# Kernel tuning notes

Hardware: AMD Instinct MI355X
Metric: run time of the kernel (lower is better)

## Reference

```python
import jax, jax.numpy as jnp
import numpy as np

SCALE = 64.0
MARGIN = 0.35
EPS = 1e-7


def setup_inputs() -> dict:
    key = jax.random.key(0)
    k1, k2, k3 = jax.random.split(key, 3)
    B, D, C = 1024, 128, 100000
    embeddings = jax.random.normal(k1, (B, D), dtype=jnp.float32)
    labels = jax.random.randint(k2, (B,), 0, C, dtype=jnp.int64)
    W = jax.random.normal(k3, (C, D), dtype=jnp.float32)
    return {"embeddings": embeddings, "labels": labels, "W": W}


def reference(embeddings, labels, W):
    # L2-normalize class weights along feature dim (torch F.normalize, p=2, dim=1)
    W_norm = W / jnp.clip(jnp.linalg.norm(W, axis=1, keepdims=True), 1e-12)
    # cosine logits [B, C]
    cos_theta = jnp.clip(embeddings @ W_norm.T, -1.0 + EPS, 1.0 - EPS)
    # subtract margin only at the target class (equivalent to one-hot scatter)
    B = cos_theta.shape[0]
    rows = jnp.arange(B)
    cos_m = cos_theta.at[rows, labels].add(-MARGIN)
    logits = SCALE * cos_m
    # softmax cross-entropy with integer labels, mean reduction
    logp = jax.nn.log_softmax(logits, axis=-1)
    nll = -logp[rows, labels]
    return jnp.mean(nll)
```

## Files before the change

### kernel.cpp

```cpp
#include <hip/hip_runtime.h>
#include <hip/hip_bf16.h>

typedef float f32x4 __attribute__((ext_vector_type(4)));

#define B_SZ 1024
#define D_SZ 128
#define C_SZ 100000
#define CPAD 100096
#define BM 128
#define BN 128
#define NG 64
#define NCT 782

#define SCALE_F   64.0f
#define MARGIN_F  0.35f
#define CLIP_F    (1.0f - 1e-7f)
#define LOG2E_F   1.4426950408889634f
#define S_LOG2E_F (64.0f * 1.4426950408889634f)

__device__ __forceinline__ void gload_lds16(const void* g, void* l) {
    __builtin_amdgcn_global_load_lds(
        (const __attribute__((address_space(1))) void*)g,
        (__attribute__((address_space(3))) void*)l, 16, 0, 0);
}

__global__ void norm_conv(const float* __restrict__ W, unsigned int* __restrict__ Wf8,
                          const float* __restrict__ E, unsigned int* __restrict__ Ef8) {
    const int b = blockIdx.x;
    if (b < 12512) {
        const int lane = threadIdx.x & 63;
        const int l32  = lane & 31;
        const int row  = b * 8 + ((threadIdx.x >> 6) << 1) + (lane >> 5);
        if (row < C_SZ) {
            float4 v = reinterpret_cast<const float4*>(W + (size_t)row * D_SZ)[l32];
            float ss = v.x * v.x + v.y * v.y + v.z * v.z + v.w * v.w;
            #pragma unroll
            for (int m = 1; m < 32; m <<= 1) ss += __shfl_xor(ss, m);
            float sc = 1.0f / fmaxf(sqrtf(ss), 1e-12f);
            int r = __builtin_amdgcn_cvt_pk_fp8_f32(v.x * sc, v.y * sc, 0, false);
            r     = __builtin_amdgcn_cvt_pk_fp8_f32(v.z * sc, v.w * sc, r, true);
            Wf8[(size_t)row * 32 + l32] = (unsigned int)r;
        } else {
            Wf8[(size_t)row * 32 + l32] = 0u;
        }
    } else {
        const int i = (b - 12512) * 256 + threadIdx.x;
        float4 v = reinterpret_cast<const float4*>(E)[i];
        int r = __builtin_amdgcn_cvt_pk_fp8_f32(v.x, v.y, 0, false);
        r     = __builtin_amdgcn_cvt_pk_fp8_f32(v.z, v.w, r, true);
        Ef8[i] = (unsigned int)r;
    }
}

__launch_bounds__(512, 3)
__global__ void gemm_lse(const unsigned char* __restrict__ Ef8,
                         const unsigned char* __restrict__ Wf8,
                         float* __restrict__ P) {
    __shared__ unsigned char sB[2][BN * D_SZ];
    __shared__ float rs[2][BM];

    const int tid  = threadIdx.x;
    const int wave = tid >> 6;
    const int lane = tid & 63;
    const int g4   = lane >> 4;
    const int l15  = lane & 15;
    const int wm   = wave >> 1;
    const int wn   = wave & 1;
    const int g    = blockIdx.x;
    const int bi   = blockIdx.y;

    const int T = (NCT - g + NG - 1) / NG;

    const char* wbase = reinterpret_cast<const char*>(Wf8);
    const int srcOff = ((tid >> 3) << 7) + ((((tid & 7) ^ ((tid >> 3) & 7))) << 4);
    const int ldsOff = wave << 10;

#define STAGE(TI, BUF)                                                         \
    {                                                                          \
        const char* _s = wbase + (size_t)(TI) * 16384 + srcOff;                \
        char* _d = reinterpret_cast<char*>(BUF) + ldsOff;                      \
        gload_lds16(_s,        _d);                                            \
        gload_lds16(_s + 8192, _d + 8192);                                     \
    }

    STAGE(g, sB[0]);

    long a[2][4];
    {
        const char* ebase = reinterpret_cast<const char*>(Ef8) + (size_t)bi * BM * 128;
        #pragma unroll
        for (int mi = 0; mi < 2; ++mi) {
            const char* pr = ebase + (wm * 32 + mi * 16 + l15) * 128 + g4 * 8;
            #pragma unroll
            for (int kk = 0; kk < 4; ++kk)
                a[mi][kk] = *reinterpret_cast<const long*>(pr + kk * 32);
        }
    }

    const int swz = (l15 & 7) << 4;
    int rowb[4];
    #pragma unroll
    for (int ni = 0; ni < 4; ++ni) rowb[ni] = (wn * 64 + ni * 16 + l15) << 7;
    int kb[4];
    #pragma unroll
    for (int kk = 0; kk < 4; ++kk) kb[kk] = (kk * 32 + g4 * 8) ^ swz;

    float rowsum[2][4] = {};

    __syncthreads();

    int cur = 0;
    for (int t = 0; t < T; ++t) {
        if (t + 1 < T) STAGE(g + (t + 1) * NG, sB[cur ^ 1]);

        const char* sBb = reinterpret_cast<const char*>(sB[cur]);
        f32x4 acc[2][4] = {};
        #pragma unroll
        for (int kk = 0; kk < 4; ++kk) {
            long b[4];
            #pragma unroll
            for (int ni = 0; ni < 4; ++ni)
                b[ni] = *reinterpret_cast<const long*>(sBb + rowb[ni] + kb[kk]);
            #pragma unroll
            for (int mi = 0; mi < 2; ++mi)
                #pragma unroll
                for (int ni = 0; ni < 4; ++ni)
                    acc[mi][ni] = __builtin_amdgcn_mfma_f32_16x16x32_fp8_fp8(
                        a[mi][kk], b[ni], acc[mi][ni], 0, 0, 0);
        }

        #pragma unroll
        for (int mi = 0; mi < 2; ++mi) {
            #pragma unroll
            for (int r = 0; r < 4; ++r) {
                float s0 = 0.0f;
                #pragma unroll
                for (int ni = 0; ni < 4; ++ni)
                    s0 += __builtin_amdgcn_exp2f(
                        fminf(fmaf(acc[mi][ni][r], S_LOG2E_F, -S_LOG2E_F), 0.0f));
                rowsum[mi][r] += s0;
            }
        }
        __syncthreads();
        cur ^= 1;
    }

    #pragma unroll
    for (int mi = 0; mi < 2; ++mi) {
        #pragma unroll
        for (int r = 0; r < 4; ++r) {
            float s = rowsum[mi][r];
            s += __shfl_xor(s, 1);
            s += __shfl_xor(s, 2);
            s += __shfl_xor(s, 4);
            s += __shfl_xor(s, 8);
            rowsum[mi][r] = s;
        }
    }
    if (l15 == 0) {
        #pragma unroll
        for (int mi = 0; mi < 2; ++mi)
            #pragma unroll
            for (int r = 0; r < 4; ++r)
                rs[wn][wm * 32 + mi * 16 + g4 * 4 + r] = rowsum[mi][r];
    }
    __syncthreads();
    if (tid < BM)
        P[(size_t)g * B_SZ + bi * BM + tid] = rs[0][tid] + rs[1][tid];
#undef STAGE
}

__global__ void row_fin(const float* __restrict__ P, const float* __restrict__ E,
                        const float* __restrict__ W, const int* __restrict__ lab,
                        float* __restrict__ nll) {
    __shared__ float red[256];
    __shared__ float red2[128];
    const int row = blockIdx.x;
    const int t   = threadIdx.x;

    red[t] = (t < NG) ? P[(size_t)t * B_SZ + row] : 0.0f;
    __syncthreads();
    #pragma unroll
    for (int off = 128; off > 0; off >>= 1) {
        if (t < off) red[t] += red[t + off];
        __syncthreads();
    }
    const float S = red[0];
    __syncthreads();

    const int lb = lab[row];
    if (t < 128) {
        const float w = W[(size_t)lb * D_SZ + t];
        const float e = E[(size_t)row * D_SZ + t];
        red[t]  = e * w;
        red2[t] = w * w;
    } else {
        red[t] = 0.0f;
    }
    __syncthreads();
    #pragma unroll
    for (int off = 64; off > 0; off >>= 1) {
        if (t < off) { red[t] += red[t + off]; red2[t] += red2[t + off]; }
        __syncthreads();
    }

    if (t == 0) {
        const float ct = red[0] / fmaxf(sqrtf(red2[0]), 1e-12f);
        const float cc = fminf(fmaxf(ct, -CLIP_F), CLIP_F);
        const float lt = SCALE_F * (cc - MARGIN_F);
        float Sadj = S - exp2f(fminf((SCALE_F * cc - SCALE_F) * LOG2E_F, 0.0f))
                       + exp2f((lt - SCALE_F) * LOG2E_F);
        nll[row] = SCALE_F + logf(Sadj) - lt;
    }
}

__global__ void mean_k(const float* __restrict__ nll, float* __restrict__ out) {
    __shared__ float part[16];
    const int t = threadIdx.x;
    float v = nll[t];
    #pragma unroll
    for (int m = 1; m < 64; m <<= 1) v += __shfl_xor(v, m);
    if ((t & 63) == 0) part[t >> 6] = v;
    __syncthreads();
    if (t < 16) {
        float u = part[t];
        #pragma unroll
        for (int m = 1; m < 16; m <<= 1) u += __shfl_xor(u, m);
        if (t == 0) out[0] = u * (1.0f / 1024.0f);
    }
}

extern "C" void kernel_launch(void* const* d_in, const int* in_sizes, int n_in,
                              void* d_out, int out_size, void* d_ws, size_t ws_size,
                              hipStream_t stream) {
    const float* E   = (const float*)d_in[0];
    const int*   lab = (const int*)d_in[1];
    const float* W   = (const float*)d_in[2];
    float*       out = (float*)d_out;

    char* ws = (char*)d_ws;
    unsigned int* Ef8 = (unsigned int*)ws;
    unsigned int* Wf8 = (unsigned int*)(ws + 131072);
    float*        P   = (float*)(ws + 131072 + 12812288);
    float*        nll = (float*)(ws + 131072 + 12812288 + 262144);

    norm_conv<<<dim3(12640),   256, 0, stream>>>(W, Wf8, E, Ef8);
    gemm_lse <<<dim3(NG, 8),   512, 0, stream>>>((const unsigned char*)Ef8,
                                                 (const unsigned char*)Wf8, P);
    row_fin  <<<dim3(B_SZ),    256, 0, stream>>>(P, E, W, lab, nll);
    mean_k   <<<dim3(1),      1024, 0, stream>>>(nll, out);
}
```

Measured before the change: 52.73 us.

## Double GEMM row tile to 256 and fold mean into row_fin via atomicAdd

Each gemm_lse block now covers 256 embedding rows instead of 128, using two sets of A fragments and accumulators. Each staged fp8 W tile therefore feeds twice as many MFMAs, and the W stream is re-read half as many times. NG doubles to 128 so the grid keeps enough blocks. The separate mean kernel is removed: out is zeroed in norm_conv and row_fin atomically adds each scaled nll, saving one launch at the cost of a nondeterministic summation order. The doubled accumulator and A-fragment state raises register pressure under the 512x3 launch bounds, which risks spills or lower occupancy.

```diff
diff --git a/kernel.cpp b/kernel.cpp
--- a/kernel.cpp
+++ b/kernel.cpp
@@ -7,9 +7,9 @@
 #define D_SZ 128
 #define C_SZ 100000
 #define CPAD 100096
-#define BM 128
+#define BM 256
 #define BN 128
-#define NG 64
+#define NG 128
 #define NCT 782
 
 #define SCALE_F   64.0f
@@ -25,7 +25,8 @@
 }
 
 __global__ void norm_conv(const float* __restrict__ W, unsigned int* __restrict__ Wf8,
-                          const float* __restrict__ E, unsigned int* __restrict__ Ef8) {
+                          const float* __restrict__ E, unsigned int* __restrict__ Ef8,
+                          float* __restrict__ out) {
     const int b = blockIdx.x;
     if (b < 12512) {
         const int lane = threadIdx.x & 63;
@@ -44,6 +45,7 @@
             Wf8[(size_t)row * 32 + l32] = 0u;
         }
     } else {
+        if (b == 12512 && threadIdx.x == 0) out[0] = 0.0f;
         const int i = (b - 12512) * 256 + threadIdx.x;
         float4 v = reinterpret_cast<const float4*>(E)[i];
         int r = __builtin_amdgcn_cvt_pk_fp8_f32(v.x, v.y, 0, false);
@@ -85,16 +87,18 @@
 
     STAGE(g, sB[0]);
 
-    long a[2][4];
+    long a[2][2][4];
     {
         const char* ebase = reinterpret_cast<const char*>(Ef8) + (size_t)bi * BM * 128;
         #pragma unroll
-        for (int mi = 0; mi < 2; ++mi) {
-            const char* pr = ebase + (wm * 32 + mi * 16 + l15) * 128 + g4 * 8;
-            #pragma unroll
-            for (int kk = 0; kk < 4; ++kk)
-                a[mi][kk] = *reinterpret_cast<const long*>(pr + kk * 32);
-        }
+        for (int h = 0; h < 2; ++h)
+            #pragma unroll
+            for (int mi = 0; mi < 2; ++mi) {
+                const char* pr = ebase + (h * 128 + wm * 32 + mi * 16 + l15) * 128 + g4 * 8;
+                #pragma unroll
+                for (int kk = 0; kk < 4; ++kk)
+                    a[h][mi][kk] = *reinterpret_cast<const long*>(pr + kk * 32);
+            }
     }
 
     const int swz = (l15 & 7) << 4;
@@ -105,7 +109,7 @@
     #pragma unroll
     for (int kk = 0; kk < 4; ++kk) kb[kk] = (kk * 32 + g4 * 8) ^ swz;
 
-    float rowsum[2][4] = {};
+    float rowsum[2][2][4] = {};
 
     __syncthreads();
 
@@ -114,7 +118,7 @@
         if (t + 1 < T) STAGE(g + (t + 1) * NG, sB[cur ^ 1]);
 
         const char* sBb = reinterpret_cast<const char*>(sB[cur]);
-        f32x4 acc[2][4] = {};
+        f32x4 acc[2][2][4] = {};
         #pragma unroll
         for (int kk = 0; kk < 4; ++kk) {
             long b[4];
@@ -122,47 +126,54 @@
             for (int ni = 0; ni < 4; ++ni)
                 b[ni] = *reinterpret_cast<const long*>(sBb + rowb[ni] + kb[kk]);
             #pragma unroll
+            for (int h = 0; h < 2; ++h)
+                #pragma unroll
+                for (int mi = 0; mi < 2; ++mi)
+                    #pragma unroll
+                    for (int ni = 0; ni < 4; ++ni)
+                        acc[h][mi][ni] = __builtin_amdgcn_mfma_f32_16x16x32_fp8_fp8(
+                            a[h][mi][kk], b[ni], acc[h][mi][ni], 0, 0, 0);
+        }
+
+        #pragma unroll
+        for (int h = 0; h < 2; ++h)
+            #pragma unroll
             for (int mi = 0; mi < 2; ++mi)
                 #pragma unroll
-                for (int ni = 0; ni < 4; ++ni)
-                    acc[mi][ni] = __builtin_amdgcn_mfma_f32_16x16x32_fp8_fp8(
-                        a[mi][kk], b[ni], acc[mi][ni], 0, 0, 0);
-        }
-
-        #pragma unroll
-        for (int mi = 0; mi < 2; ++mi) {
-            #pragma unroll
-            for (int r = 0; r < 4; ++r) {
-                float s0 = 0.0f;
-                #pragma unroll
-                for (int ni = 0; ni < 4; ++ni)
-                    s0 += __builtin_amdgcn_exp2f(
-                        fminf(fmaf(acc[mi][ni][r], S_LOG2E_F, -S_LOG2E_F), 0.0f));
-                rowsum[mi][r] += s0;
-            }
-        }
+                for (int r = 0; r < 4; ++r) {
+                    float s0 = 0.0f;
+                    #pragma unroll
+                    for (int ni = 0; ni < 4; ++ni)
+                        s0 += __builtin_amdgcn_exp2f(
+                            fminf(fmaf(acc[h][mi][ni][r], S_LOG2E_F, -S_LOG2E_F), 0.0f));
+                    rowsum[h][mi][r] += s0;
+                }
+
         __syncthreads();
         cur ^= 1;
     }
 
     #pragma unroll
-    for (int mi = 0; mi < 2; ++mi) {
-        #pragma unroll
-        for (int r = 0; r < 4; ++r) {
-            float s = rowsum[mi][r];
-            s += __shfl_xor(s, 1);
-            s += __shfl_xor(s, 2);
-            s += __shfl_xor(s, 4);
-            s += __shfl_xor(s, 8);
-            rowsum[mi][r] = s;
-        }
-    }
+    for (int h = 0; h < 2; ++h)
+        #pragma unroll
+        for (int mi = 0; mi < 2; ++mi)
+            #pragma unroll
+            for (int r = 0; r < 4; ++r) {
+                float s = rowsum[h][mi][r];
+                s += __shfl_xor(s, 1);
+                s += __shfl_xor(s, 2);
+                s += __shfl_xor(s, 4);
+                s += __shfl_xor(s, 8);
+                rowsum[h][mi][r] = s;
+            }
     if (l15 == 0) {
         #pragma unroll
-        for (int mi = 0; mi < 2; ++mi)
-            #pragma unroll
-            for (int r = 0; r < 4; ++r)
-                rs[wn][wm * 32 + mi * 16 + g4 * 4 + r] = rowsum[mi][r];
+        for (int h = 0; h < 2; ++h)
+            #pragma unroll
+            for (int mi = 0; mi < 2; ++mi)
+                #pragma unroll
+                for (int r = 0; r < 4; ++r)
+                    rs[wn][h * 128 + wm * 32 + mi * 16 + g4 * 4 + r] = rowsum[h][mi][r];
     }
     __syncthreads();
     if (tid < BM)
@@ -172,7 +183,7 @@
 
 __global__ void row_fin(const float* __restrict__ P, const float* __restrict__ E,
                         const float* __restrict__ W, const int* __restrict__ lab,
-                        float* __restrict__ nll) {
+                        float* __restrict__ out) {
     __shared__ float red[256];
     __shared__ float red2[128];
     const int row = blockIdx.x;
@@ -210,23 +221,7 @@
         const float lt = SCALE_F * (cc - MARGIN_F);
         float Sadj = S - exp2f(fminf((SCALE_F * cc - SCALE_F) * LOG2E_F, 0.0f))
                        + exp2f((lt - SCALE_F) * LOG2E_F);
-        nll[row] = SCALE_F + logf(Sadj) - lt;
-    }
-}
-
-__global__ void mean_k(const float* __restrict__ nll, float* __restrict__ out) {
-    __shared__ float part[16];
-    const int t = threadIdx.x;
-    float v = nll[t];
-    #pragma unroll
-    for (int m = 1; m < 64; m <<= 1) v += __shfl_xor(v, m);
-    if ((t & 63) == 0) part[t >> 6] = v;
-    __syncthreads();
-    if (t < 16) {
-        float u = part[t];
-        #pragma unroll
-        for (int m = 1; m < 16; m <<= 1) u += __shfl_xor(u, m);
-        if (t == 0) out[0] = u * (1.0f / 1024.0f);
+        atomicAdd(out, (SCALE_F + logf(Sadj) - lt) * (1.0f / 1024.0f));
     }
 }
 
@@ -242,11 +237,9 @@
     unsigned int* Ef8 = (unsigned int*)ws;
     unsigned int* Wf8 = (unsigned int*)(ws + 131072);
     float*        P   = (float*)(ws + 131072 + 12812288);
-    float*        nll = (float*)(ws + 131072 + 12812288 + 262144);
-
-    norm_conv<<<dim3(12640),   256, 0, stream>>>(W, Wf8, E, Ef8);
-    gemm_lse <<<dim3(NG, 8),   512, 0, stream>>>((const unsigned char*)Ef8,
+
+    norm_conv<<<dim3(12640),   256, 0, stream>>>(W, Wf8, E, Ef8, out);
+    gemm_lse <<<dim3(NG, 4),   512, 0, stream>>>((const unsigned char*)Ef8,
                                                  (const unsigned char*)Wf8, P);
-    row_fin  <<<dim3(B_SZ),    256, 0, stream>>>(P, E, W, lab, nll);
-    mean_k   <<<dim3(1),      1024, 0, stream>>>(nll, out);
-}
+    row_fin  <<<dim3(B_SZ),    256, 0, stream>>>(P, E, W, lab, out);
+}
```

Result: slower. 70.23 us (+33.2%).
